# Optimization experiments

Hardware: AMD Instinct MI355X
Metric: run time of the kernel (lower is better)

## Reference

```python
import jax, jax.numpy as jnp
import numpy as np

N_HEAD, D_MODEL, D_HEAD = 16, 1024, 64
SCALE = 1.0 / (D_HEAD ** 0.5)
LN_EPS = 1e-5


def _rel_shift(x):
    # x: [b, n, i, j] -> Transformer-XL relative shift
    b, n, i, j = x.shape
    zero_pad = jnp.zeros((b, n, i, 1), x.dtype)
    x_padded = jnp.concatenate([zero_pad, x], axis=3).reshape(b, n, j + 1, i)
    return x_padded[:, :, 1:, :].reshape(b, n, i, j)


def setup_inputs() -> dict:
    key = jax.random.key(0)
    ks = jax.random.split(key, 16)
    qlen, bsz, mem_len = 1024, 2, 1024
    klen = qlen + mem_len
    rlen = klen
    s = 0.02
    inp = {
        'w': jax.random.normal(ks[0], (qlen, bsz, D_MODEL), jnp.float32),
        'r': jax.random.normal(ks[1], (rlen, D_MODEL), jnp.float32),
        'mems': jax.random.normal(ks[2], (mem_len, bsz, D_MODEL), jnp.float32),
        'r_w_bias': s * jax.random.normal(ks[3], (N_HEAD, D_HEAD), jnp.float32),
        'r_r_bias': s * jax.random.normal(ks[4], (N_HEAD, D_HEAD), jnp.float32),
        # causal mask with memory offset: position i attends to j <= i + mem_len
        'attn_mask': jnp.triu(jnp.ones((qlen, klen), bool), k=1 + mem_len),
        'Wq': s * jax.random.normal(ks[5], (D_MODEL, N_HEAD * D_HEAD), jnp.float32),
        'bq': jnp.zeros((N_HEAD * D_HEAD,), jnp.float32),
        'Wk': s * jax.random.normal(ks[6], (D_MODEL, N_HEAD * D_HEAD), jnp.float32),
        'bk': jnp.zeros((N_HEAD * D_HEAD,), jnp.float32),
        'Wv': s * jax.random.normal(ks[7], (D_MODEL, N_HEAD * D_HEAD), jnp.float32),
        'bv': jnp.zeros((N_HEAD * D_HEAD,), jnp.float32),
        'Wr': s * jax.random.normal(ks[8], (D_MODEL, N_HEAD * D_HEAD), jnp.float32),
        'br': jnp.zeros((N_HEAD * D_HEAD,), jnp.float32),
        'Wo': s * jax.random.normal(ks[9], (N_HEAD * D_HEAD, D_MODEL), jnp.float32),
        'bo': jnp.zeros((D_MODEL,), jnp.float32),
        'ln_g': jnp.ones((D_MODEL,), jnp.float32),
        'ln_b': jnp.zeros((D_MODEL,), jnp.float32),
    }
    return inp


def reference(w, r, mems, r_w_bias, r_r_bias, Wq, bq, Wk, bk, Wv, bv, Wr, br, Wo, bo, ln_g, ln_b, attn_mask):
    qlen, bsz, _ = w.shape
    cat = jnp.concatenate([mems, w], axis=0)                      # [klen, b, d_model]
    klen = cat.shape[0]
    q = (cat @ Wq + bq)[-qlen:].reshape(qlen, bsz, N_HEAD, D_HEAD)
    k = (cat @ Wk + bk).reshape(klen, bsz, N_HEAD, D_HEAD)
    v = (cat @ Wv + bv).reshape(klen, bsz, N_HEAD, D_HEAD)
    rk = (r @ Wr + br).reshape(-1, N_HEAD, D_HEAD)               # [rlen, n, d]

    AC = jnp.einsum('ibnd,jbnd->bnij', q + r_w_bias, k)          # content term
    BD = _rel_shift(jnp.einsum('ibnd,jnd->bnij', q + r_r_bias, rk))  # relative term
    attn_score = SCALE * (AC + BD)                                # [b, n, i, j]
    attn_score = jnp.where(attn_mask[None, None, :, :], -jnp.inf, attn_score)
    attn_prob = jax.nn.softmax(attn_score, axis=3)
    attn_vec = jnp.einsum('bnij,jbnd->ibnd', attn_prob, v).reshape(qlen, bsz, N_HEAD * D_HEAD)
    attn_out = attn_vec @ Wo + bo

    res = w + attn_out                                            # post-LN (pre_lnorm=False)
    mu = jnp.mean(res, axis=-1, keepdims=True)
    var = jnp.var(res, axis=-1, keepdims=True)
    return (res - mu) / jnp.sqrt(var + LN_EPS) * ln_g + ln_b
```

## Files before the change

### kernel.cpp

```cpp
#include <hip/hip_runtime.h>
#include <math.h>

#define N_HEADC 16
#define D_MODELC 1024
#define D_HEADC 64
#define QLENC 1024
#define BSZC 2
#define MEMLENC 1024
#define KLENC 2048
#define SCALEC 0.125f
#define SL2C 0.18033688011112042f
#define LN_EPSC 1e-5f
#define RINGC 192

typedef __attribute__((ext_vector_type(8))) short short8;
typedef __attribute__((ext_vector_type(4))) float f32x4;

#define MFMA16(a, b, c) __builtin_amdgcn_mfma_f32_16x16x32_bf16((a), (b), (c), 0, 0, 0)

__device__ inline unsigned short f2bf(float x) {
    union { float f; unsigned int u; } c; c.f = x;
    unsigned int r = c.u + 0x7FFFu + ((c.u >> 16) & 1u);
    return (unsigned short)(r >> 16);
}
__device__ inline unsigned int pk2(float a, float b) {
    union { float f; unsigned int u; } x, y; x.f = a; y.f = b;
    return (x.u >> 16) | (y.u & 0xFFFF0000u);
}
__device__ inline float bf2f(short s) {
    union { unsigned int u; float f; } c; c.u = ((unsigned int)(unsigned short)s) << 16;
    return c.f;
}
__device__ inline float asf(unsigned u) {
    union { unsigned int u; float f; } c; c.u = u; return c.f;
}

__device__ __forceinline__ void load_lds16(const short* g, short* l) {
    __builtin_amdgcn_global_load_lds(
        (const __attribute__((address_space(1))) void*)g,
        (__attribute__((address_space(3))) void*)l,
        16, 0, 0);
}

__global__ __launch_bounds__(256) void prep_kernel(
    const float* __restrict__ mems, const float* __restrict__ wIn,
    const float* __restrict__ rIn,
    const float* __restrict__ W0, const float* __restrict__ W1,
    const float* __restrict__ W2, const float* __restrict__ W3,
    const float* __restrict__ W4,
    short* __restrict__ cat_bf, short* __restrict__ r_bf,
    short* __restrict__ D0, short* __restrict__ D1, short* __restrict__ D2,
    short* __restrict__ D3, short* __restrict__ D4)
{
    __shared__ short tile[64][72];
    const int z = blockIdx.z;
    const int t = threadIdx.x;

    if (z >= 5) {
        int lb = (z - 5) * 256 + blockIdx.y * 16 + blockIdx.x;
        int idx = (lb * 256 + t) * 8;
        const float* src; short* dst;
        if (idx < 4194304) {
            src = (idx < 2097152) ? (mems + idx) : (wIn + idx - 2097152);
            dst = cat_bf + idx;
        } else {
            src = rIn + (idx - 4194304);
            dst = r_bf + (idx - 4194304);
        }
        short8 o;
        #pragma unroll
        for (int e = 0; e < 8; ++e) o[e] = (short)f2bf(src[e]);
        *(short8*)dst = o;
        return;
    }

    const float* W; short* D;
    switch (z) {
        case 0: W = W0; D = D0; break;
        case 1: W = W1; D = D1; break;
        case 2: W = W2; D = D2; break;
        case 3: W = W3; D = D3; break;
        default: W = W4; D = D4; break;
    }
    const int n0 = blockIdx.x * 64, k0 = blockIdx.y * 64;
    #pragma unroll
    for (int it = 0; it < 2; ++it) {
        int idx = t + it * 256;
        int kl = idx >> 3, c8 = idx & 7;
        const float* src = W + (size_t)(k0 + kl) * D_MODELC + n0 + c8 * 8;
        short8 s;
        #pragma unroll
        for (int e = 0; e < 8; ++e) s[e] = (short)f2bf(src[e]);
        *(short8*)&tile[kl][c8 * 8] = s;
    }
    __syncthreads();
    #pragma unroll
    for (int it = 0; it < 2; ++it) {
        int idx = t + it * 256;
        int nl = idx >> 3, c8 = idx & 7;
        short8 s;
        #pragma unroll
        for (int e = 0; e < 8; ++e) s[e] = tile[c8 * 8 + e][nl];
        *(short8*)(D + (size_t)(n0 + nl) * D_MODELC + k0 + c8 * 8) = s;
    }
}

__global__ __launch_bounds__(256) void vtrans_kernel(
    const short* __restrict__ v_bf, short* __restrict__ vt)
{
    __shared__ short tile[64][72];
    const int t = threadIdx.x;
    const int j0 = blockIdx.x * 64;
    const int bn = blockIdx.y;
    const int b = bn & 1, n = bn >> 1;
    #pragma unroll
    for (int it = 0; it < 2; ++it) {
        int idx = t + it * 256;
        int jl = idx >> 3, c8 = idx & 7;
        short8 s = *(const short8*)(v_bf + ((size_t)(j0 + jl) * 2 + b) * D_MODELC + n * 64 + c8 * 8);
        *(short8*)&tile[jl][c8 * 8] = s;
    }
    __syncthreads();
    #pragma unroll
    for (int it = 0; it < 2; ++it) {
        int idx = t + it * 256;
        int dl = idx >> 3, c8 = idx & 7;
        short8 s;
        #pragma unroll
        for (int e = 0; e < 8; ++e) s[e] = tile[c8 * 8 + e][dl];
        *(short8*)(vt + ((size_t)(b * 16 + n) * 64 + dl) * (size_t)KLENC + j0 + c8 * 8) = s;
    }
}

__global__ __launch_bounds__(256, 3) void proj_gemm_kernel(
    const short* __restrict__ cat, const short* __restrict__ rin,
    const short* __restrict__ WqT, const short* __restrict__ WkT,
    const short* __restrict__ WvT, const short* __restrict__ WrT,
    const float* __restrict__ bq, const float* __restrict__ bk,
    const float* __restrict__ bv, const float* __restrict__ br,
    const float* __restrict__ rwb, const float* __restrict__ rrb,
    short* __restrict__ qw, short* __restrict__ qr,
    short* __restrict__ kb, short* __restrict__ vb, short* __restrict__ rk)
{
    __shared__ short As[128][32];
    __shared__ short Bs[128][32];

    const int lin = blockIdx.y * 8 + blockIdx.x;
    const int sw  = (lin & 7) * 96 + (lin >> 3);
    const int bx  = sw & 7;
    const int by  = sw >> 3;

    const short* A; const short* Bt; const float* bias; int yt, mode;
    if (by < 32)      { A = cat;                         Bt = WkT; bias = bk; yt = by;      mode = 0; }
    else if (by < 64) { A = cat;                         Bt = WvT; bias = bv; yt = by - 32; mode = 1; }
    else if (by < 80) { A = cat + (size_t)2048 * 1024;   Bt = WqT; bias = bq; yt = by - 64; mode = 2; }
    else              { A = rin;                         Bt = WrT; bias = br; yt = by - 80; mode = 3; }

    const int row0 = yt * 128, col0 = bx * 128;
    const int t = threadIdx.x;
    const int lane = t & 63, wid = t >> 6;
    const int row16 = lane & 15, g8 = lane >> 4;
    const int wr = wid >> 1, wc = wid & 1;

    f32x4 acc[4][4];
    #pragma unroll
    for (int m = 0; m < 4; ++m)
        #pragma unroll
        for (int nn = 0; nn < 4; ++nn)
            acc[m][nn] = (f32x4){0.f, 0.f, 0.f, 0.f};

    short* AsB = &As[0][0] + wid * 1024;
    short* BsB = &Bs[0][0] + wid * 1024;
    const int srow4 = lane >> 2;
    const int cs4 = (lane & 3) ^ ((lane >> 3) & 3);
    const short* Ag = A  + (size_t)(row0 + wid * 32 + srow4) * D_MODELC + cs4 * 8;
    const short* Bg = Bt + (size_t)(col0 + wid * 32 + srow4) * D_MODELC + cs4 * 8;
    const int xc2 = (row16 >> 1) & 3;

    for (int k0 = 0; k0 < D_MODELC; k0 += 32) {
        load_lds16(Ag + k0,              AsB);
        load_lds16(Ag + k0 + 16 * 1024,  AsB + 512);
        load_lds16(Bg + k0,              BsB);
        load_lds16(Bg + k0 + 16 * 1024,  BsB + 512);
        __syncthreads();
        short8 af[4], bfr[4];
        #pragma unroll
        for (int m = 0; m < 4; ++m)
            af[m] = *(const short8*)&As[wr * 64 + m * 16 + row16][(g8 ^ xc2) * 8];
        #pragma unroll
        for (int nn = 0; nn < 4; ++nn)
            bfr[nn] = *(const short8*)&Bs[wc * 64 + nn * 16 + row16][(g8 ^ xc2) * 8];
        #pragma unroll
        for (int m = 0; m < 4; ++m)
            #pragma unroll
            for (int nn = 0; nn < 4; ++nn)
                acc[m][nn] = MFMA16(af[m], bfr[nn], acc[m][nn]);
        __syncthreads();
    }

    float bvv[4], w1[4], w2[4];
    #pragma unroll
    for (int nn = 0; nn < 4; ++nn) {
        int c = col0 + wc * 64 + nn * 16 + row16;
        bvv[nn] = bias[c];
        w1[nn] = rwb[c];
        w2[nn] = rrb[c];
    }
    if (mode == 2) {
        #pragma unroll
        for (int m = 0; m < 4; ++m)
            #pragma unroll
            for (int nn = 0; nn < 4; ++nn) {
                int c = col0 + wc * 64 + nn * 16 + row16;
                #pragma unroll
                for (int reg = 0; reg < 4; ++reg) {
                    int r = row0 + wr * 64 + m * 16 + g8 * 4 + reg;
                    float v = acc[m][nn][reg] + bvv[nn];
                    qw[(size_t)r * D_MODELC + c] = (short)f2bf((v + w1[nn]) * SL2C);
                    qr[(size_t)r * D_MODELC + c] = (short)f2bf((v + w2[nn]) * SL2C);
                }
            }
    } else {
        short* C = (mode == 0) ? kb : (mode == 1) ? vb : rk;
        #pragma unroll
        for (int m = 0; m < 4; ++m)
            #pragma unroll
            for (int nn = 0; nn < 4; ++nn) {
                int c = col0 + wc * 64 + nn * 16 + row16;
                #pragma unroll
                for (int reg = 0; reg < 4; ++reg) {
                    int r = row0 + wr * 64 + m * 16 + g8 * 4 + reg;
                    C[(size_t)r * D_MODELC + c] = (short)f2bf(acc[m][nn][reg] + bvv[nn]);
                }
            }
    }
}

__global__ __launch_bounds__(256, 3) void wo_gemm_kernel(
    const short* __restrict__ A, const short* __restrict__ Bt,
    short* __restrict__ out0, short* __restrict__ out1)
{
    __shared__ short As[128][32];
    __shared__ short Bs[128][32];
    const int kz = blockIdx.z;
    short* C = kz ? out1 : out0;
    const int row0 = blockIdx.y * 128, col0 = blockIdx.x * 128;
    const int t = threadIdx.x;
    const int lane = t & 63, wid = t >> 6;
    const int row16 = lane & 15, g8 = lane >> 4;
    const int wr = wid >> 1, wc = wid & 1;

    f32x4 acc[4][4];
    #pragma unroll
    for (int m = 0; m < 4; ++m)
        #pragma unroll
        for (int nn = 0; nn < 4; ++nn)
            acc[m][nn] = (f32x4){0.f, 0.f, 0.f, 0.f};

    short* AsB = &As[0][0] + wid * 1024;
    short* BsB = &Bs[0][0] + wid * 1024;
    const int srow4 = lane >> 2;
    const int cs4 = (lane & 3) ^ ((lane >> 3) & 3);
    const short* Ag = A  + (size_t)(row0 + wid * 32 + srow4) * D_MODELC + cs4 * 8;
    const short* Bg = Bt + (size_t)(col0 + wid * 32 + srow4) * D_MODELC + cs4 * 8;
    const int xc2 = (row16 >> 1) & 3;

    const int kbase = kz * 512;
    for (int k0 = kbase; k0 < kbase + 512; k0 += 32) {
        load_lds16(Ag + k0,             AsB);
        load_lds16(Ag + k0 + 16 * 1024, AsB + 512);
        load_lds16(Bg + k0,             BsB);
        load_lds16(Bg + k0 + 16 * 1024, BsB + 512);
        __syncthreads();
        short8 af[4], bfr[4];
        #pragma unroll
        for (int m = 0; m < 4; ++m)
            af[m] = *(const short8*)&As[wr * 64 + m * 16 + row16][(g8 ^ xc2) * 8];
        #pragma unroll
        for (int nn = 0; nn < 4; ++nn)
            bfr[nn] = *(const short8*)&Bs[wc * 64 + nn * 16 + row16][(g8 ^ xc2) * 8];
        #pragma unroll
        for (int m = 0; m < 4; ++m)
            #pragma unroll
            for (int nn = 0; nn < 4; ++nn)
                acc[m][nn] = MFMA16(af[m], bfr[nn], acc[m][nn]);
        __syncthreads();
    }

    #pragma unroll
    for (int m = 0; m < 4; ++m)
        #pragma unroll
        for (int nn = 0; nn < 4; ++nn) {
            int c = col0 + wc * 64 + nn * 16 + row16;
            #pragma unroll
            for (int reg = 0; reg < 4; ++reg) {
                int r = row0 + wr * 64 + m * 16 + g8 * 4 + reg;
                C[(size_t)r * D_MODELC + c] = (short)f2bf(acc[m][nn][reg]);
            }
        }
}

__global__ __launch_bounds__(256, 2) void attn_mfma_kernel(
    const short* __restrict__ qw, const short* __restrict__ qr,
    const short* __restrict__ kb, const short* __restrict__ rkb,
    const short* __restrict__ vt, short* __restrict__ av)
{
    __shared__ short Kl[2][64][64];
    __shared__ short Vl[2][64][64];
    __shared__ short Rl[RINGC][64];
    __shared__ short pun[4][1376];
    __shared__ float scb[4][16];

    const int wave = threadIdx.x >> 6, lane = threadIdx.x & 63;
    const int row16 = lane & 15, g8 = lane >> 4;
    const int srow = lane >> 3, chk = lane & 7;
    const int swz = srow & 7;

    const int lin = blockIdx.y * 16 + blockIdx.x;
    const int xcd = lin & 7;
    const int u   = lin >> 3;
    const int v   = u & 31;
    const int bn  = xcd * 4 + (v >> 3);
    const int tt  = v & 7;
    const int ic  = (u >> 5) ? (15 - tt) : tt;
    const int b = bn & 1, n = bn >> 1;
    const int i0 = ic * 64;
    const int i0w = i0 + wave * 16;

    short8 qwf[2], qrf[2];
    #pragma unroll
    for (int ks = 0; ks < 2; ++ks) {
        size_t off = ((size_t)(i0w + row16) * 2 + b) * D_MODELC + n * 64 + ks * 32 + g8 * 8;
        qwf[ks] = *(const short8*)(qw + off);
        qrf[ks] = *(const short8*)(qr + off);
    }

    #pragma unroll
    for (int t = 0; t < 2; ++t) {
        int rr = wave * 16 + t * 8;
        int j  = rr + srow;
        int cs = chk ^ swz;
        load_lds16(kb + ((size_t)j * 2 + b) * D_MODELC + n * 64 + cs * 8, &Kl[0][rr][0]);
        load_lds16(vt + ((size_t)((b * 16 + n) * 64 + rr + srow)) * KLENC + cs * 8,
                   &Vl[0][rr][0]);
    }
    {
        const int p0 = 960 - i0;
        #pragma unroll
        for (int t = 0; t < 4; ++t) {
            int jrb_ = p0 + wave * 32 + t * 8;
            int slotb = jrb_ % RINGC;
            int jr = jrb_ + srow;
            int jc = jr < KLENC ? jr : KLENC - 1;
            int cs = chk ^ swz;
            load_lds16(rkb + (size_t)jc * D_MODELC + n * 64 + cs * 8, &Rl[slotb][0]);
        }
    }

    f32x4 accO[4];
    #pragma unroll
    for (int dt = 0; dt < 4; ++dt) accO[dt] = (f32x4){0.f, 0.f, 0.f, 0.f};
    float m = -INFINITY;
    float lsum = 0.f;

    const int T = (i0 + 63 + MEMLENC + 64) >> 6;
    const int r7 = row16 & 7;
    const int off15 = 15 - row16;
    const int kal = off15 & ~3;
    const unsigned ksh = (unsigned)(off15 & 3) * 16;

    __syncthreads();

    #pragma unroll 2
    for (int s = 0; s < T; ++s) {
        const int j0 = s * 64;
        const int cur = s & 1;
        const int nxt = cur ^ 1;
        const bool stage = (s + 1 < T);

        if (stage) {
            #pragma unroll
            for (int t = 0; t < 2; ++t) {
                int rr = wave * 16 + t * 8;
                int j  = j0 + 64 + rr + srow;
                if (j > KLENC - 1) j = KLENC - 1;
                int cs = chk ^ swz;
                load_lds16(kb + ((size_t)j * 2 + b) * D_MODELC + n * 64 + cs * 8, &Kl[nxt][rr][0]);
            }
            {
                const int nb = j0 + 1088 - i0;
                #pragma unroll
                for (int t = 0; t < 2; ++t) {
                    int jrb_ = nb + wave * 16 + t * 8;
                    int slotb = jrb_ % RINGC;
                    int jr = jrb_ + srow;
                    int jc = jr < KLENC ? jr : KLENC - 1;
                    int cs = chk ^ swz;
                    load_lds16(rkb + (size_t)jc * D_MODELC + n * 64 + cs * 8, &Rl[slotb][0]);
                }
            }
            {
                const int jsrc = (j0 + 64 <= KLENC - 64) ? (j0 + 64) : (KLENC - 64);
                #pragma unroll
                for (int t = 0; t < 2; ++t) {
                    int rr = wave * 16 + t * 8;
                    int cs = chk ^ swz;
                    load_lds16(vt + ((size_t)((b * 16 + n) * 64 + rr + srow)) * KLENC + jsrc + cs * 8,
                               &Vl[nxt][rr][0]);
                }
            }
        }

        __builtin_amdgcn_s_setprio(1);
        f32x4 st[4];
        #pragma unroll
        for (int jt = 0; jt < 4; ++jt) {
            st[jt] = (f32x4){0.f, 0.f, 0.f, 0.f};
            const short* kr = &Kl[cur][jt * 16 + row16][0];
            st[jt] = MFMA16(*(const short8*)(kr + ((g8 ^ r7) * 8)),       qwf[0], st[jt]);
            st[jt] = MFMA16(*(const short8*)(kr + (((4 + g8) ^ r7) * 8)), qwf[1], st[jt]);
        }

        const int jrb_w = j0 - i0w + 1008;
        const int sb = jrb_w % RINGC;
        short* bdT = &pun[wave][0];
        #pragma unroll
        for (int rt = 0; rt < 5; ++rt) {
            int rsl = sb + rt * 16 + row16;
            if (rsl >= RINGC) rsl -= RINGC;
            const short* rr = &Rl[rsl][0];
            f32x4 bd = (f32x4){0.f, 0.f, 0.f, 0.f};
            bd = MFMA16(*(const short8*)(rr + ((g8 ^ r7) * 8)),       qrf[0], bd);
            bd = MFMA16(*(const short8*)(rr + (((4 + g8) ^ r7) * 8)), qrf[1], bd);
            uint2 wv;
            wv.x = pk2(bd[0], bd[1]);
            wv.y = pk2(bd[2], bd[3]);
            *(uint2*)&bdT[row16 * 84 + rt * 16 + g8 * 4] = wv;
        }
        __builtin_amdgcn_s_setprio(0);

        float sl[4][4];
        {
            const bool tail = !(j0 + 63 <= i0w + MEMLENC);
            #pragma unroll
            for (int jt = 0; jt < 4; ++jt) {
                const unsigned* pwd = (const unsigned*)&bdT[row16 * 84 + jt * 16 + g8 * 4 + kal];
                uint2 wa = *(const uint2*)pwd;
                uint2 wb = *(const uint2*)(pwd + 2);
                unsigned s0 = (ksh < 32) ? wa.x : wa.y;
                unsigned s1 = (ksh < 32) ? wa.y : wb.x;
                unsigned s2 = (ksh < 32) ? wb.x : wb.y;
                unsigned sh2 = ksh & 31;
                unsigned lo = (unsigned)(((((unsigned long long)s1) << 32) | s0) >> sh2);
                unsigned hi = (unsigned)(((((unsigned long long)s2) << 32) | s1) >> sh2);
                float b0 = asf(lo << 16), b1 = asf(lo & 0xffff0000u);
                float b2 = asf(hi << 16), b3 = asf(hi & 0xffff0000u);
                sl[jt][0] = st[jt][0] + b0;
                sl[jt][1] = st[jt][1] + b1;
                sl[jt][2] = st[jt][2] + b2;
                sl[jt][3] = st[jt][3] + b3;
                if (tail) {
                    #pragma unroll
                    for (int reg = 0; reg < 4; ++reg) {
                        const int jl = jt * 16 + g8 * 4 + reg;
                        if (j0 + jl > i0w + row16 + MEMLENC) sl[jt][reg] = -INFINITY;
                    }
                }
            }
        }

        float mx0 = fmaxf(fmaxf(sl[0][0], sl[0][1]), fmaxf(sl[0][2], sl[0][3]));
        float mx1 = fmaxf(fmaxf(sl[1][0], sl[1][1]), fmaxf(sl[1][2], sl[1][3]));
        float mx2 = fmaxf(fmaxf(sl[2][0], sl[2][1]), fmaxf(sl[2][2], sl[2][3]));
        float mx3 = fmaxf(fmaxf(sl[3][0], sl[3][1]), fmaxf(sl[3][2], sl[3][3]));
        float mx = fmaxf(fmaxf(mx0, mx1), fmaxf(mx2, mx3));

        if (__any(mx > m + 8.f)) {
            float mxr = mx;
            mxr = fmaxf(mxr, __shfl_xor(mxr, 16, 64));
            mxr = fmaxf(mxr, __shfl_xor(mxr, 32, 64));
            float mn = fmaxf(m, mxr);
            float sc = exp2f(m - mn);
            m = mn;
            lsum *= sc;
            if (lane < 16) scb[wave][lane] = sc;
            float4 s4 = *(const float4*)&scb[wave][g8 * 4];
            #pragma unroll
            for (int dt = 0; dt < 4; ++dt) {
                accO[dt][0] *= s4.x; accO[dt][1] *= s4.y;
                accO[dt][2] *= s4.z; accO[dt][3] *= s4.w;
            }
        }

        #pragma unroll
        for (int jt = 0; jt < 4; ++jt)
            #pragma unroll
            for (int reg = 0; reg < 4; ++reg)
                sl[jt][reg] = exp2f(sl[jt][reg] - m);
        float ps = ((sl[0][0] + sl[0][1]) + (sl[0][2] + sl[0][3]))
                 + ((sl[1][0] + sl[1][1]) + (sl[1][2] + sl[1][3]))
                 + ((sl[2][0] + sl[2][1]) + (sl[2][2] + sl[2][3]))
                 + ((sl[3][0] + sl[3][1]) + (sl[3][2] + sl[3][3]));
        short* pP = &pun[wave][0];
        #pragma unroll
        for (int jt = 0; jt < 4; ++jt) {
            const int ch = (jt * 2 + (g8 >> 1)) ^ r7;
            uint2 pkd;
            pkd.x = pk2(sl[jt][0], sl[jt][1]);
            pkd.y = pk2(sl[jt][2], sl[jt][3]);
            *(uint2*)&pP[row16 * 64 + ch * 8 + (g8 & 1) * 4] = pkd;
        }
        lsum += ps;

        __builtin_amdgcn_s_setprio(1);
        #pragma unroll
        for (int ks2 = 0; ks2 < 2; ++ks2) {
            short8 pf = *(const short8*)&pP[row16 * 64 + (((ks2 * 4 + g8) ^ r7) * 8)];
            #pragma unroll
            for (int dt = 0; dt < 4; ++dt) {
                const short* vp = &Vl[cur][dt * 16 + row16][(((ks2 * 4 + g8) ^ r7) * 8)];
                accO[dt] = MFMA16(pf, *(const short8*)vp, accO[dt]);
            }
        }
        __builtin_amdgcn_s_setprio(0);

        if (stage) __syncthreads();
    }

    lsum += __shfl_xor(lsum, 16, 64);
    lsum += __shfl_xor(lsum, 32, 64);
    if (lane < 16) scb[wave][lane] = lsum;
    float4 l4 = *(const float4*)&scb[wave][g8 * 4];
    float rl4[4] = {1.f / l4.x, 1.f / l4.y, 1.f / l4.z, 1.f / l4.w};
    #pragma unroll
    for (int dt = 0; dt < 4; ++dt)
        #pragma unroll
        for (int reg = 0; reg < 4; ++reg) {
            size_t o = ((size_t)(i0w + g8 * 4 + reg) * 2 + b) * D_MODELC + n * 64 + dt * 16 + row16;
            av[o] = (short)f2bf(accO[dt][reg] * rl4[reg]);
        }
}

__global__ __launch_bounds__(256) void ln_kernel(
    const float* __restrict__ w, const short* __restrict__ p0,
    const short* __restrict__ p1, const float* __restrict__ bo,
    const float* __restrict__ g, const float* __restrict__ bb,
    float* __restrict__ out)
{
    __shared__ float red[2][4];
    const int row = blockIdx.x;
    const int lane = threadIdx.x & 63;
    const int wv = threadIdx.x >> 6;
    const size_t base = (size_t)row * D_MODELC;
    const int c = threadIdx.x * 4;

    float4 xw = *(const float4*)&w[base + c];
    ushort4 a0 = *(const ushort4*)&p0[base + c];
    ushort4 a1 = *(const ushort4*)&p1[base + c];
    float4 xb = *(const float4*)&bo[c];
    float x[4] = {xw.x + bf2f((short)a0.x) + bf2f((short)a1.x) + xb.x,
                  xw.y + bf2f((short)a0.y) + bf2f((short)a1.y) + xb.y,
                  xw.z + bf2f((short)a0.z) + bf2f((short)a1.z) + xb.z,
                  xw.w + bf2f((short)a0.w) + bf2f((short)a1.w) + xb.w};

    float sum = x[0] + x[1] + x[2] + x[3];
    float ssq = x[0]*x[0] + x[1]*x[1] + x[2]*x[2] + x[3]*x[3];
    #pragma unroll
    for (int off = 32; off > 0; off >>= 1) {
        sum += __shfl_xor(sum, off, 64);
        ssq += __shfl_xor(ssq, off, 64);
    }
    if (lane == 0) { red[0][wv] = sum; red[1][wv] = ssq; }
    __syncthreads();
    sum = red[0][0] + red[0][1] + red[0][2] + red[0][3];
    ssq = red[1][0] + red[1][1] + red[1][2] + red[1][3];

    const float mu = sum * (1.0f / D_MODELC);
    const float var = ssq * (1.0f / D_MODELC) - mu * mu;
    const float rstd = rsqrtf(var + LN_EPSC);

    float4 o;
    o.x = (x[0] - mu) * rstd * g[c] + bb[c];
    o.y = (x[1] - mu) * rstd * g[c+1] + bb[c+1];
    o.z = (x[2] - mu) * rstd * g[c+2] + bb[c+2];
    o.w = (x[3] - mu) * rstd * g[c+3] + bb[c+3];
    *(float4*)&out[base + c] = o;
}

extern "C" void kernel_launch(void* const* d_in, const int* in_sizes, int n_in,
                              void* d_out, int out_size, void* d_ws, size_t ws_size,
                              hipStream_t stream)
{
    const float* w    = (const float*)d_in[0];
    const float* r    = (const float*)d_in[1];
    const float* mems = (const float*)d_in[2];
    const float* rwb  = (const float*)d_in[3];
    const float* rrb  = (const float*)d_in[4];
    const float* Wq = (const float*)d_in[6];
    const float* bq = (const float*)d_in[7];
    const float* Wk = (const float*)d_in[8];
    const float* bk = (const float*)d_in[9];
    const float* Wv = (const float*)d_in[10];
    const float* bv = (const float*)d_in[11];
    const float* Wr = (const float*)d_in[12];
    const float* br = (const float*)d_in[13];
    const float* Wo = (const float*)d_in[14];
    const float* bo = (const float*)d_in[15];
    const float* ln_g = (const float*)d_in[16];
    const float* ln_b = (const float*)d_in[17];
    float* out = (float*)d_out;

    char* ws = (char*)d_ws;
    const size_t MB = 1ull << 20;
    short* cat_bf = (short*)(ws + 0 * MB);
    short* r_bf   = (short*)(ws + 8 * MB);
    short* Wq_t   = (short*)(ws + 12 * MB);
    short* Wk_t   = (short*)(ws + 14 * MB);
    short* Wv_t   = (short*)(ws + 16 * MB);
    short* Wr_t   = (short*)(ws + 18 * MB);
    short* Wo_t   = (short*)(ws + 20 * MB);
    short* qw_bf  = (short*)(ws + 22 * MB);
    short* qr_bf  = (short*)(ws + 26 * MB);
    short* k_bf   = (short*)(ws + 30 * MB);
    short* v_bf   = (short*)(ws + 38 * MB);
    short* rk_bf  = (short*)(ws + 46 * MB);
    short* vt     = (short*)(ws + 50 * MB);
    short* av_bf  = (short*)(ws + 58 * MB);
    short* wo0    = Wq_t;
    short* wo1    = Wv_t;

    dim3 blk(256);

    prep_kernel<<<dim3(16, 16, 17), blk, 0, stream>>>(
        mems, w, r, Wq, Wk, Wv, Wr, Wo,
        cat_bf, r_bf, Wq_t, Wk_t, Wv_t, Wr_t, Wo_t);

    proj_gemm_kernel<<<dim3(8, 96), blk, 0, stream>>>(
        cat_bf, r_bf, Wq_t, Wk_t, Wv_t, Wr_t,
        bq, bk, bv, br, rwb, rrb,
        qw_bf, qr_bf, k_bf, v_bf, rk_bf);

    vtrans_kernel<<<dim3(32, 32), blk, 0, stream>>>(v_bf, vt);

    attn_mfma_kernel<<<dim3(16, 32), blk, 0, stream>>>(
        qw_bf, qr_bf, k_bf, rk_bf, vt, av_bf);

    wo_gemm_kernel<<<dim3(8, 16, 2), blk, 0, stream>>>(av_bf, Wo_t, wo0, wo1);

    ln_kernel<<<dim3(2048), blk, 0, stream>>>(w, wo0, wo1, bo, ln_g, ln_b, out);
}
```

Before: 138.4 us.

## Double-buffer LDS tiles in projection and output GEMMs to overlap loads with MFMA

The projection and Wo GEMM kernels now keep two LDS buffers for A and B tiles. Each iteration prefetches the next k-slice into the alternate buffer while MFMAs consume the current one, and needs only one barrier per iteration instead of two. MFMA sections are also wrapped in s_setprio to raise wave priority during compute. LDS use per block doubles (32 KB), which may limit the 3-blocks-per-CU occupancy target. Correctness depends on load_lds16 completing before the single barrier.

```diff
diff --git a/kernel.cpp b/kernel.cpp
--- a/kernel.cpp
+++ b/kernel.cpp
@@ -142,8 +142,8 @@
     short* __restrict__ qw, short* __restrict__ qr,
     short* __restrict__ kb, short* __restrict__ vb, short* __restrict__ rk)
 {
-    __shared__ short As[128][32];
-    __shared__ short Bs[128][32];
+    __shared__ short As[2][128][32];
+    __shared__ short Bs[2][128][32];
 
     const int lin = blockIdx.y * 8 + blockIdx.x;
     const int sw  = (lin & 7) * 96 + (lin >> 3);
@@ -169,33 +169,42 @@
         for (int nn = 0; nn < 4; ++nn)
             acc[m][nn] = (f32x4){0.f, 0.f, 0.f, 0.f};
 
-    short* AsB = &As[0][0] + wid * 1024;
-    short* BsB = &Bs[0][0] + wid * 1024;
     const int srow4 = lane >> 2;
     const int cs4 = (lane & 3) ^ ((lane >> 3) & 3);
     const short* Ag = A  + (size_t)(row0 + wid * 32 + srow4) * D_MODELC + cs4 * 8;
     const short* Bg = Bt + (size_t)(col0 + wid * 32 + srow4) * D_MODELC + cs4 * 8;
     const int xc2 = (row16 >> 1) & 3;
 
-    for (int k0 = 0; k0 < D_MODELC; k0 += 32) {
-        load_lds16(Ag + k0,              AsB);
-        load_lds16(Ag + k0 + 16 * 1024,  AsB + 512);
-        load_lds16(Bg + k0,              BsB);
-        load_lds16(Bg + k0 + 16 * 1024,  BsB + 512);
-        __syncthreads();
+    load_lds16(Ag,             &As[0][0][0] + wid * 1024);
+    load_lds16(Ag + 16 * 1024, &As[0][0][0] + wid * 1024 + 512);
+    load_lds16(Bg,             &Bs[0][0][0] + wid * 1024);
+    load_lds16(Bg + 16 * 1024, &Bs[0][0][0] + wid * 1024 + 512);
+    __syncthreads();
+
+    for (int kk = 0; kk < 32; ++kk) {
+        const int cb = kk & 1, nb = cb ^ 1;
+        if (kk < 31) {
+            int k0n = (kk + 1) * 32;
+            load_lds16(Ag + k0n,             &As[nb][0][0] + wid * 1024);
+            load_lds16(Ag + k0n + 16 * 1024, &As[nb][0][0] + wid * 1024 + 512);
+            load_lds16(Bg + k0n,             &Bs[nb][0][0] + wid * 1024);
+            load_lds16(Bg + k0n + 16 * 1024, &Bs[nb][0][0] + wid * 1024 + 512);
+        }
         short8 af[4], bfr[4];
         #pragma unroll
         for (int m = 0; m < 4; ++m)
-            af[m] = *(const short8*)&As[wr * 64 + m * 16 + row16][(g8 ^ xc2) * 8];
+            af[m] = *(const short8*)&As[cb][wr * 64 + m * 16 + row16][(g8 ^ xc2) * 8];
         #pragma unroll
         for (int nn = 0; nn < 4; ++nn)
-            bfr[nn] = *(const short8*)&Bs[wc * 64 + nn * 16 + row16][(g8 ^ xc2) * 8];
+            bfr[nn] = *(const short8*)&Bs[cb][wc * 64 + nn * 16 + row16][(g8 ^ xc2) * 8];
+        __builtin_amdgcn_s_setprio(1);
         #pragma unroll
         for (int m = 0; m < 4; ++m)
             #pragma unroll
             for (int nn = 0; nn < 4; ++nn)
                 acc[m][nn] = MFMA16(af[m], bfr[nn], acc[m][nn]);
-        __syncthreads();
+        __builtin_amdgcn_s_setprio(0);
+        if (kk < 31) __syncthreads();
     }
 
     float bvv[4], w1[4], w2[4];
@@ -240,8 +249,8 @@
     const short* __restrict__ A, const short* __restrict__ Bt,
     short* __restrict__ out0, short* __restrict__ out1)
 {
-    __shared__ short As[128][32];
-    __shared__ short Bs[128][32];
+    __shared__ short As[2][128][32];
+    __shared__ short Bs[2][128][32];
     const int kz = blockIdx.z;
     short* C = kz ? out1 : out0;
     const int row0 = blockIdx.y * 128, col0 = blockIdx.x * 128;
@@ -257,34 +266,43 @@
         for (int nn = 0; nn < 4; ++nn)
             acc[m][nn] = (f32x4){0.f, 0.f, 0.f, 0.f};
 
-    short* AsB = &As[0][0] + wid * 1024;
-    short* BsB = &Bs[0][0] + wid * 1024;
     const int srow4 = lane >> 2;
     const int cs4 = (lane & 3) ^ ((lane >> 3) & 3);
-    const short* Ag = A  + (size_t)(row0 + wid * 32 + srow4) * D_MODELC + cs4 * 8;
-    const short* Bg = Bt + (size_t)(col0 + wid * 32 + srow4) * D_MODELC + cs4 * 8;
+    const int kbase = kz * 512;
+    const short* Ag = A  + (size_t)(row0 + wid * 32 + srow4) * D_MODELC + kbase + cs4 * 8;
+    const short* Bg = Bt + (size_t)(col0 + wid * 32 + srow4) * D_MODELC + kbase + cs4 * 8;
     const int xc2 = (row16 >> 1) & 3;
 
-    const int kbase = kz * 512;
-    for (int k0 = kbase; k0 < kbase + 512; k0 += 32) {
-        load_lds16(Ag + k0,             AsB);
-        load_lds16(Ag + k0 + 16 * 1024, AsB + 512);
-        load_lds16(Bg + k0,             BsB);
-        load_lds16(Bg + k0 + 16 * 1024, BsB + 512);
-        __syncthreads();
+    load_lds16(Ag,             &As[0][0][0] + wid * 1024);
+    load_lds16(Ag + 16 * 1024, &As[0][0][0] + wid * 1024 + 512);
+    load_lds16(Bg,             &Bs[0][0][0] + wid * 1024);
+    load_lds16(Bg + 16 * 1024, &Bs[0][0][0] + wid * 1024 + 512);
+    __syncthreads();
+
+    for (int kk = 0; kk < 16; ++kk) {
+        const int cb = kk & 1, nb = cb ^ 1;
+        if (kk < 15) {
+            int k0n = (kk + 1) * 32;
+            load_lds16(Ag + k0n,             &As[nb][0][0] + wid * 1024);
+            load_lds16(Ag + k0n + 16 * 1024, &As[nb][0][0] + wid * 1024 + 512);
+            load_lds16(Bg + k0n,             &Bs[nb][0][0] + wid * 1024);
+            load_lds16(Bg + k0n + 16 * 1024, &Bs[nb][0][0] + wid * 1024 + 512);
+        }
         short8 af[4], bfr[4];
         #pragma unroll
         for (int m = 0; m < 4; ++m)
-            af[m] = *(const short8*)&As[wr * 64 + m * 16 + row16][(g8 ^ xc2) * 8];
+            af[m] = *(const short8*)&As[cb][wr * 64 + m * 16 + row16][(g8 ^ xc2) * 8];
         #pragma unroll
         for (int nn = 0; nn < 4; ++nn)
-            bfr[nn] = *(const short8*)&Bs[wc * 64 + nn * 16 + row16][(g8 ^ xc2) * 8];
+            bfr[nn] = *(const short8*)&Bs[cb][wc * 64 + nn * 16 + row16][(g8 ^ xc2) * 8];
+        __builtin_amdgcn_s_setprio(1);
         #pragma unroll
         for (int m = 0; m < 4; ++m)
             #pragma unroll
             for (int nn = 0; nn < 4; ++nn)
                 acc[m][nn] = MFMA16(af[m], bfr[nn], acc[m][nn]);
-        __syncthreads();
+        __builtin_amdgcn_s_setprio(0);
+        if (kk < 15) __syncthreads();
     }
 
     #pragma unroll
```

After: 138.8 us. No clear change (+0.3%).
